# Optimization experiments

Measured on AMD Instinct MI355X. Metric: run time of the kernel, lower is better.

The kernel has to match this reference:

```python
import jax, jax.numpy as jnp
import numpy as np

B, T, D, U, C = 128, 256, 512, 1024, 10

def setup_inputs() -> dict:
    key = jax.random.key(0)
    ks = jax.random.split(key, 5)
    scale_in = 1.0 / np.sqrt(D)
    scale_rec = 1.0 / np.sqrt(U)
    return {
        "x": jax.random.normal(ks[0], (B, T, D), dtype=jnp.float32),
        "kernel": jax.random.normal(ks[1], (D, 4 * U), dtype=jnp.float32) * scale_in,
        "recurrent_kernel": jax.random.normal(ks[2], (U, 4 * U), dtype=jnp.float32) * scale_rec,
        "bias": jnp.zeros((4 * U,), dtype=jnp.float32),
        "w_cls": jax.random.normal(ks[3], (U, C), dtype=jnp.float32) * scale_rec,
        "b_cls": jnp.zeros((C,), dtype=jnp.float32),
    }

def _lstm_forward(x, kernel, recurrent_kernel, bias, w_cls, b_cls):
    # x: [B, T, D]. Keras LSTMCell gate order: i, f, g (candidate), o.
    # Precompute input projections for all timesteps in one big GEMM: [B,T,4U]
    xz = jnp.einsum('btd,dg->btg', x, kernel) + bias
    u = recurrent_kernel.shape[0]
    h0 = jnp.zeros((x.shape[0], u), dtype=x.dtype)
    c0 = jnp.zeros((x.shape[0], u), dtype=x.dtype)

    def step(carry, zt):
        h, c = carry
        z = zt + h @ recurrent_kernel          # [B, 4U]
        i, f, g, o = jnp.split(z, 4, axis=-1)
        i = jax.nn.sigmoid(i)
        f = jax.nn.sigmoid(f)
        o = jax.nn.sigmoid(o)
        c_new = f * c + i * jnp.tanh(g)
        h_new = o * jnp.tanh(c_new)
        return (h_new, c_new), None

    (h_last, _), _ = jax.lax.scan(step, (h0, c0), jnp.swapaxes(xz, 0, 1))
    logits = h_last @ w_cls + b_cls
    return jax.nn.softmax(logits, axis=-1)

def reference(x, kernel, recurrent_kernel, bias, w_cls, b_cls):
    return _lstm_forward(x, kernel, recurrent_kernel, bias, w_cls, b_cls)
```

## Files before the change

### kernel.cpp

```cpp
#include <hip/hip_runtime.h>

typedef unsigned short u16;
typedef unsigned int u32;
typedef unsigned long long u64;
typedef __attribute__((ext_vector_type(8))) short bf16x8;
typedef __attribute__((ext_vector_type(8))) unsigned short u16x8;
typedef __attribute__((ext_vector_type(4))) float f32x4;

#define TC 32
#define NCHUNK 8

static __device__ __forceinline__ u16 f2bf(float x) {
  union { float f; u32 u; } v; v.f = x;
  u32 r = v.u + 0x7fffu + ((v.u >> 16) & 1u);
  return (u16)(r >> 16);
}
static __device__ __forceinline__ float bf2f(u16 h) {
  union { u32 u; float f; } v; v.u = ((u32)h) << 16;
  return v.f;
}
static __device__ __forceinline__ float sigm(float x) {
  return 1.0f / (1.0f + __expf(-x));
}
static __device__ __forceinline__ void gload_lds16(const u16* g, u16* l) {
  __builtin_amdgcn_global_load_lds(
      (const __attribute__((address_space(1))) void*)g,
      (__attribute__((address_space(3))) void*)l, 16, 0, 0);
}

__global__ __launch_bounds__(256) void conv_x_kernel(const float* __restrict__ x,
                                                     u16* __restrict__ xh,
                                                     u16* __restrict__ xl) {
  int idx = blockIdx.x * 256 + threadIdx.x;
  size_t i8 = (size_t)idx * 8;
  int b = (int)(i8 >> 17);
  int r = (int)(i8 & 131071);
  int t = r >> 9;
  int d = r & 511;
  const f32x4* s = (const f32x4*)(x + i8);
  f32x4 v0 = s[0], v1 = s[1];
  u16x8 vh, vl;
#pragma unroll
  for (int j = 0; j < 8; ++j) {
    float v = (j < 4) ? v0[j] : v1[j - 4];
    u16 h = f2bf(v);
    vh[j] = h;
    vl[j] = f2bf(v - bf2f(h));
  }
  size_t o = ((size_t)(t * 128 + b)) * 512 + d;
  *(u16x8*)(xh + o) = vh;
  *(u16x8*)(xl + o) = vl;
}

__global__ __launch_bounds__(256) void tsplit_kernel(const float* __restrict__ w,
                                                     u16* __restrict__ oh,
                                                     u16* __restrict__ ol, int K) {
  int idx = blockIdx.x * 256 + threadIdx.x;
  int d = idx >> 10;
  int g4 = (idx & 1023) * 4;
  f32x4 v = *(const f32x4*)(w + (size_t)d * 4096 + g4);
#pragma unroll
  for (int j = 0; j < 4; ++j) {
    int g = g4 + j;
    u16 h = f2bf(v[j]);
    oh[(size_t)g * K + d] = h;
    ol[(size_t)g * K + d] = f2bf(v[j] - bf2f(h));
  }
}

__global__ __launch_bounds__(256) void gemm1_kernel(const u16* __restrict__ xh,
                                                    const u16* __restrict__ xl,
                                                    const u16* __restrict__ kh,
                                                    const u16* __restrict__ kl,
                                                    const float* __restrict__ bias,
                                                    float* __restrict__ xz, int c) {
  __shared__ u16 Ah[4096], Al[4096], Bh[4096], Bl[4096];
  const int tid = threadIdx.x;
  const int w = tid >> 6, l = tid & 63;
  const int m0w = blockIdx.y * 128;
  const int m0g = c * 4096 + m0w;
  const int n0 = blockIdx.x * 128;
  const int wr = w >> 1, wc = w & 1;
  const int srow = l >> 2, schunk = l & 3;
  const int fr = l & 15, fc = l >> 4;

  f32x4 acc[4][4];
#pragma unroll
  for (int a = 0; a < 4; ++a)
#pragma unroll
    for (int b = 0; b < 4; ++b) acc[a][b] = (f32x4){0.f, 0.f, 0.f, 0.f};

  for (int kt = 0; kt < 16; ++kt) {
    const int koff = kt * 32 + schunk * 8;
#pragma unroll
    for (int i = 0; i < 8; ++i) {
      const int q = w + i * 4;
      const int buf = q >> 3, ch = q & 7;
      const size_t ro = (size_t)(ch * 16 + srow);
      if (buf == 0)      gload_lds16(xh + (m0g + ro) * 512 + koff, Ah + ch * 512);
      else if (buf == 1) gload_lds16(xl + (m0g + ro) * 512 + koff, Al + ch * 512);
      else if (buf == 2) gload_lds16(kh + (n0 + ro) * 512 + koff, Bh + ch * 512);
      else               gload_lds16(kl + (n0 + ro) * 512 + koff, Bl + ch * 512);
    }
    __syncthreads();

    bf16x8 a_h[4], a_l[4], b_h[4], b_l[4];
#pragma unroll
    for (int mf = 0; mf < 4; ++mf) {
      int row = wr * 64 + mf * 16 + fr;
      a_h[mf] = *(const bf16x8*)(Ah + row * 32 + fc * 8);
      a_l[mf] = *(const bf16x8*)(Al + row * 32 + fc * 8);
    }
#pragma unroll
    for (int nf = 0; nf < 4; ++nf) {
      int col = wc * 64 + nf * 16 + fr;
      b_h[nf] = *(const bf16x8*)(Bh + col * 32 + fc * 8);
      b_l[nf] = *(const bf16x8*)(Bl + col * 32 + fc * 8);
    }
#pragma unroll
    for (int mf = 0; mf < 4; ++mf)
#pragma unroll
      for (int nf = 0; nf < 4; ++nf) {
        acc[mf][nf] = __builtin_amdgcn_mfma_f32_16x16x32_bf16(a_h[mf], b_h[nf], acc[mf][nf], 0, 0, 0);
        acc[mf][nf] = __builtin_amdgcn_mfma_f32_16x16x32_bf16(a_h[mf], b_l[nf], acc[mf][nf], 0, 0, 0);
        acc[mf][nf] = __builtin_amdgcn_mfma_f32_16x16x32_bf16(a_l[mf], b_h[nf], acc[mf][nf], 0, 0, 0);
      }
    __syncthreads();
  }

#pragma unroll
  for (int nf = 0; nf < 4; ++nf) {
    const int col = n0 + wc * 64 + nf * 16 + fr;
    const float bv = bias[col];
#pragma unroll
    for (int mf = 0; mf < 4; ++mf) {
      const int rw = m0w + wr * 64 + mf * 16 + fc * 4;
#pragma unroll
      for (int rg = 0; rg < 4; ++rg)
        xz[(size_t)(rw + rg) * 4096 + col] = acc[mf][nf][rg] + bv;
    }
  }
}

__global__ __launch_bounds__(256) void init_kernel(u32* flags) {
  for (int i = threadIdx.x; i < 4352; i += 256) flags[i] = 0u;
}

__global__ __launch_bounds__(256, 1) void lstm_scan_kernel(
    const float* __restrict__ xz,
    const u16* __restrict__ rwh, const u16* __restrict__ rwl,
    u32* __restrict__ h32, float* __restrict__ cf,
    u32* __restrict__ flags, int c) {
  __shared__ u16 Rh[32768];
  __shared__ u16 Rl[32768];
  const int tid = threadIdx.x;
  const int w = tid >> 6, l = tid & 63;
  const int blk = blockIdx.x;
  const int mi = blk >> 7, ui = blk & 127;

  for (int gidx = tid; gidx < 4096; gidx += 256) {
    const int lr = gidx & 63;
    const int ks = (gidx >> 6) & 31;
    const int nf = gidx >> 11;
    const int cc = lr & 15;
    const int kb = ks * 32 + ((lr >> 4) << 3);
    const int gate = nf * 2 + (cc >> 3);
    const size_t gcol = (size_t)(gate * 1024 + ui * 8 + (cc & 7));
    *(u16x8*)(Rh + gidx * 8) = *(const u16x8*)(rwh + gcol * 1024 + kb);
    *(u16x8*)(Rl + gidx * 8) = *(const u16x8*)(rwl + gcol * 1024 + kb);
  }

  const int fr = l & 15, fc = l >> 4;
  const int crow = mi * 64 + w * 16 + fc * 4;
  const int uu = ui * 8 + (fr & 7);
  const int gcol0 = ((fr >> 3) ? 1024 : 0) + uu;
  const int gcol1 = ((fr >> 3) ? 3072 : 2048) + uu;

  const u32 rbase = mi * 65536 + w * 16384 + l * 8;
  const u32 wbase = mi * 65536 + w * 16384 + (u32)(ui >> 2) * 512 +
                    ((u32)(ui & 3) * 16 + (u32)(fc * 4)) * 8 + (u32)(fr & 7);

  float cs[4] = {0.f, 0.f, 0.f, 0.f};
  if (c && fr < 8) {
#pragma unroll
    for (int rg = 0; rg < 4; ++rg) cs[rg] = cf[(size_t)(crow + rg) * 1024 + uu];
  }
  __syncthreads();

  for (int tc = 0; tc < TC; ++tc) {
    const int t = c * TC + tc;
    f32x4 a0 = (f32x4){0.f, 0.f, 0.f, 0.f};
    f32x4 a1 = (f32x4){0.f, 0.f, 0.f, 0.f};
    if (t) {
      const u32* hp = h32 + ((u32)(t & 1)) * 131072u + rbase;
#pragma unroll 4
      for (int ks = 0; ks < 32; ++ks) {
        const u64* hq = (const u64*)(hp + ks * 512);
        u64 q0 = __hip_atomic_load(hq + 0, __ATOMIC_RELAXED, __HIP_MEMORY_SCOPE_AGENT);
        u64 q1 = __hip_atomic_load(hq + 1, __ATOMIC_RELAXED, __HIP_MEMORY_SCOPE_AGENT);
        u64 q2 = __hip_atomic_load(hq + 2, __ATOMIC_RELAXED, __HIP_MEMORY_SCOPE_AGENT);
        u64 q3 = __hip_atomic_load(hq + 3, __ATOMIC_RELAXED, __HIP_MEMORY_SCOPE_AGENT);
        u32 P0 = (u32)q0, P1 = (u32)(q0 >> 32);
        u32 P2 = (u32)q1, P3 = (u32)(q1 >> 32);
        u32 P4 = (u32)q2, P5 = (u32)(q2 >> 32);
        u32 P6 = (u32)q3, P7 = (u32)(q3 >> 32);
        union { u32 wv[4]; bf16x8 v; } uh, ul;
        uh.wv[0] = __builtin_amdgcn_perm(P1, P0, 0x07060302u);
        ul.wv[0] = __builtin_amdgcn_perm(P1, P0, 0x05040100u);
        uh.wv[1] = __builtin_amdgcn_perm(P3, P2, 0x07060302u);
        ul.wv[1] = __builtin_amdgcn_perm(P3, P2, 0x05040100u);
        uh.wv[2] = __builtin_amdgcn_perm(P5, P4, 0x07060302u);
        ul.wv[2] = __builtin_amdgcn_perm(P5, P4, 0x05040100u);
        uh.wv[3] = __builtin_amdgcn_perm(P7, P6, 0x07060302u);
        ul.wv[3] = __builtin_amdgcn_perm(P7, P6, 0x05040100u);
        bf16x8 b0h = *(const bf16x8*)(Rh + (ks * 64 + l) * 8);
        bf16x8 b0l = *(const bf16x8*)(Rl + (ks * 64 + l) * 8);
        bf16x8 b1h = *(const bf16x8*)(Rh + ((32 + ks) * 64 + l) * 8);
        bf16x8 b1l = *(const bf16x8*)(Rl + ((32 + ks) * 64 + l) * 8);
        a0 = __builtin_amdgcn_mfma_f32_16x16x32_bf16(uh.v, b0h, a0, 0, 0, 0);
        a0 = __builtin_amdgcn_mfma_f32_16x16x32_bf16(uh.v, b0l, a0, 0, 0, 0);
        a0 = __builtin_amdgcn_mfma_f32_16x16x32_bf16(ul.v, b0h, a0, 0, 0, 0);
        a1 = __builtin_amdgcn_mfma_f32_16x16x32_bf16(uh.v, b1h, a1, 0, 0, 0);
        a1 = __builtin_amdgcn_mfma_f32_16x16x32_bf16(uh.v, b1l, a1, 0, 0, 0);
        a1 = __builtin_amdgcn_mfma_f32_16x16x32_bf16(ul.v, b1h, a1, 0, 0, 0);
      }
    }
    const float* xzt = xz + ((size_t)tc << 19);
    float z0[4], z1[4];
#pragma unroll
    for (int rg = 0; rg < 4; ++rg) {
      z0[rg] = a0[rg] + xzt[(size_t)(crow + rg) * 4096 + gcol0];
      z1[rg] = a1[rg] + xzt[(size_t)(crow + rg) * 4096 + gcol1];
    }
    u32* wp = h32 + ((u32)((t + 1) & 1)) * 131072u + wbase;
#pragma unroll
    for (int rg = 0; rg < 4; ++rg) {
      float p0 = __shfl_xor(z0[rg], 8, 64);
      float p1 = __shfl_xor(z1[rg], 8, 64);
      if (fr < 8) {
        float ig = sigm(z0[rg]);
        float fg = sigm(p0);
        float gg = tanhf(z1[rg]);
        float og = sigm(p1);
        float cn = fg * cs[rg] + ig * gg;
        cs[rg] = cn;
        float hv = og * tanhf(cn);
        u16 hi = f2bf(hv);
        u16 lo = f2bf(hv - bf2f(hi));
        u32 P = ((u32)hi << 16) | (u32)lo;
        __hip_atomic_store(wp + rg * 8, P,
                           __ATOMIC_RELAXED, __HIP_MEMORY_SCOPE_AGENT);
      }
    }
    const u32 tgt = (u32)(t + 1);
    asm volatile("s_waitcnt vmcnt(0)" ::: "memory");
    __syncthreads();
    u32* release = flags + 4096 + mi * 16;
    if (ui == 0) {
      if (tid == 0)
        __hip_atomic_store(flags + blk * 16, tgt, __ATOMIC_RELAXED, __HIP_MEMORY_SCOPE_AGENT);
      if (tid < 128) {
        const u32* f = flags + (mi * 128 + tid) * 16;
        for (int g = 0; g < (1 << 18); ++g) {
          if (__hip_atomic_load(f, __ATOMIC_RELAXED, __HIP_MEMORY_SCOPE_AGENT) >= tgt) break;
        }
      }
      __syncthreads();
      if (tid == 0)
        __hip_atomic_store(release, tgt, __ATOMIC_RELAXED, __HIP_MEMORY_SCOPE_AGENT);
    } else {
      if (tid == 0) {
        __hip_atomic_store(flags + blk * 16, tgt, __ATOMIC_RELAXED, __HIP_MEMORY_SCOPE_AGENT);
        for (int g = 0; g < (1 << 18); ++g) {
          if (__hip_atomic_load(release, __ATOMIC_RELAXED, __HIP_MEMORY_SCOPE_AGENT) >= tgt) break;
          __builtin_amdgcn_s_sleep(1);
        }
      }
      __syncthreads();
    }
  }

  if (fr < 8) {
#pragma unroll
    for (int rg = 0; rg < 4; ++rg) cf[(size_t)(crow + rg) * 1024 + uu] = cs[rg];
  }
}

__global__ __launch_bounds__(256) void cls_kernel(const u32* __restrict__ h32,
                                                  const float* __restrict__ wcls,
                                                  const float* __restrict__ bcls,
                                                  float* __restrict__ out) {
  __shared__ float red[2560];
  const int tid = threadIdx.x;
  const int row = blockIdx.x;
  const int rmi = row >> 6, rw = (row >> 4) & 3, lr = row & 15;
  const u32 rb = (u32)rmi * 65536u + (u32)rw * 16384u;
  float acc[10];
#pragma unroll
  for (int cc = 0; cc < 10; ++cc) acc[cc] = 0.f;
  const int k0 = tid * 4;
  for (int k = k0; k < k0 + 4; ++k) {
    const int ks = k >> 5, hi2 = (k >> 3) & 3, j = k & 7;
    u32 P = h32[rb + (u32)ks * 512u + ((u32)hi2 * 16u + (u32)lr) * 8u + (u32)j];
    float hv = bf2f((u16)(P >> 16)) + bf2f((u16)(P & 0xffffu));
#pragma unroll
    for (int cc = 0; cc < 10; ++cc) acc[cc] += hv * wcls[(size_t)k * 10 + cc];
  }
#pragma unroll
  for (int cc = 0; cc < 10; ++cc) red[tid * 10 + cc] = acc[cc];
  __syncthreads();
  for (int s = 128; s >= 1; s >>= 1) {
    if (tid < s) {
#pragma unroll
      for (int cc = 0; cc < 10; ++cc) red[tid * 10 + cc] += red[(tid + s) * 10 + cc];
    }
    __syncthreads();
  }
  if (tid == 0) {
    float lg[10];
    float m = -1e30f;
#pragma unroll
    for (int cc = 0; cc < 10; ++cc) { lg[cc] = red[cc] + bcls[cc]; m = fmaxf(m, lg[cc]); }
    float ssum = 0.f;
#pragma unroll
    for (int cc = 0; cc < 10; ++cc) { lg[cc] = __expf(lg[cc] - m); ssum += lg[cc]; }
    float inv = 1.f / ssum;
#pragma unroll
    for (int cc = 0; cc < 10; ++cc) out[row * 10 + cc] = lg[cc] * inv;
  }
}

extern "C" void kernel_launch(void* const* d_in, const int* in_sizes, int n_in,
                              void* d_out, int out_size, void* d_ws, size_t ws_size,
                              hipStream_t stream) {
  const float* x    = (const float*)d_in[0];
  const float* kern = (const float*)d_in[1];
  const float* rker = (const float*)d_in[2];
  const float* bias = (const float*)d_in[3];
  const float* wcls = (const float*)d_in[4];
  const float* bcls = (const float*)d_in[5];
  float* out = (float*)d_out;
  char* ws = (char*)d_ws;

  float* xz = (float*)(ws + 0UL);
  u16* xh   = (u16*)(ws + 67108864UL);
  u16* xl   = (u16*)(ws + 100663296UL);
  u16* kh   = (u16*)(ws + 134217728UL);
  u16* kl   = (u16*)(ws + 138412032UL);
  u16* rh   = (u16*)(ws + 142606336UL);
  u16* rl   = (u16*)(ws + 150994944UL);
  u32* h32  = (u32*)(ws + 159383552UL);
  float* cf = (float*)(ws + 160432128UL);
  u32* flg  = (u32*)(ws + 160956416UL);

  conv_x_kernel<<<8192, 256, 0, stream>>>(x, xh, xl);
  tsplit_kernel<<<2048, 256, 0, stream>>>(kern, kh, kl, 512);
  tsplit_kernel<<<4096, 256, 0, stream>>>(rker, rh, rl, 1024);
  init_kernel<<<1, 256, 0, stream>>>(flg);

  for (int c = 0; c < NCHUNK; ++c) {
    gemm1_kernel<<<dim3(32, 32), 256, 0, stream>>>(xh, xl, kh, kl, bias, xz, c);
    void* sargs[7];
    int cv = c;
    sargs[0] = (void*)&xz;
    sargs[1] = (void*)&rh;
    sargs[2] = (void*)&rl;
    sargs[3] = (void*)&h32;
    sargs[4] = (void*)&cf;
    sargs[5] = (void*)&flg;
    sargs[6] = (void*)&cv;
    hipLaunchCooperativeKernel((const void*)lstm_scan_kernel, dim3(256), dim3(256),
                               sargs, 0u, stream);
  }
  cls_kernel<<<128, 256, 0, stream>>>(h32, wcls, bcls, out);
}
```

Measured before the change: 4.270 ms.

## Store hidden state as single bf16 and drop low-part recurrent MFMA

```diff
diff --git a/kernel.cpp b/kernel.cpp
--- a/kernel.cpp
+++ b/kernel.cpp
@@ -149,7 +149,7 @@
 __global__ __launch_bounds__(256, 1) void lstm_scan_kernel(
     const float* __restrict__ xz,
     const u16* __restrict__ rwh, const u16* __restrict__ rwl,
-    u32* __restrict__ h32, float* __restrict__ cf,
+    u16* __restrict__ h16, float* __restrict__ cf,
     u32* __restrict__ flags, int c) {
   __shared__ u16 Rh[32768];
   __shared__ u16 Rl[32768];
@@ -189,50 +189,40 @@
 
   for (int tc = 0; tc < TC; ++tc) {
     const int t = c * TC + tc;
+    const float* xzt = xz + ((size_t)tc << 19);
+    float xv0[4], xv1[4];
+#pragma unroll
+    for (int rg = 0; rg < 4; ++rg) {
+      xv0[rg] = xzt[(size_t)(crow + rg) * 4096 + gcol0];
+      xv1[rg] = xzt[(size_t)(crow + rg) * 4096 + gcol1];
+    }
     f32x4 a0 = (f32x4){0.f, 0.f, 0.f, 0.f};
     f32x4 a1 = (f32x4){0.f, 0.f, 0.f, 0.f};
     if (t) {
-      const u32* hp = h32 + ((u32)(t & 1)) * 131072u + rbase;
+      const u16* hp = h16 + ((u32)(t & 1)) * 131072u + rbase;
 #pragma unroll 4
       for (int ks = 0; ks < 32; ++ks) {
         const u64* hq = (const u64*)(hp + ks * 512);
-        u64 q0 = __hip_atomic_load(hq + 0, __ATOMIC_RELAXED, __HIP_MEMORY_SCOPE_AGENT);
-        u64 q1 = __hip_atomic_load(hq + 1, __ATOMIC_RELAXED, __HIP_MEMORY_SCOPE_AGENT);
-        u64 q2 = __hip_atomic_load(hq + 2, __ATOMIC_RELAXED, __HIP_MEMORY_SCOPE_AGENT);
-        u64 q3 = __hip_atomic_load(hq + 3, __ATOMIC_RELAXED, __HIP_MEMORY_SCOPE_AGENT);
-        u32 P0 = (u32)q0, P1 = (u32)(q0 >> 32);
-        u32 P2 = (u32)q1, P3 = (u32)(q1 >> 32);
-        u32 P4 = (u32)q2, P5 = (u32)(q2 >> 32);
-        u32 P6 = (u32)q3, P7 = (u32)(q3 >> 32);
-        union { u32 wv[4]; bf16x8 v; } uh, ul;
-        uh.wv[0] = __builtin_amdgcn_perm(P1, P0, 0x07060302u);
-        ul.wv[0] = __builtin_amdgcn_perm(P1, P0, 0x05040100u);
-        uh.wv[1] = __builtin_amdgcn_perm(P3, P2, 0x07060302u);
-        ul.wv[1] = __builtin_amdgcn_perm(P3, P2, 0x05040100u);
-        uh.wv[2] = __builtin_amdgcn_perm(P5, P4, 0x07060302u);
-        ul.wv[2] = __builtin_amdgcn_perm(P5, P4, 0x05040100u);
-        uh.wv[3] = __builtin_amdgcn_perm(P7, P6, 0x07060302u);
-        ul.wv[3] = __builtin_amdgcn_perm(P7, P6, 0x05040100u);
+        union { u64 q[2]; bf16x8 v; } ah;
+        ah.q[0] = __hip_atomic_load(hq + 0, __ATOMIC_RELAXED, __HIP_MEMORY_SCOPE_AGENT);
+        ah.q[1] = __hip_atomic_load(hq + 1, __ATOMIC_RELAXED, __HIP_MEMORY_SCOPE_AGENT);
         bf16x8 b0h = *(const bf16x8*)(Rh + (ks * 64 + l) * 8);
         bf16x8 b0l = *(const bf16x8*)(Rl + (ks * 64 + l) * 8);
         bf16x8 b1h = *(const bf16x8*)(Rh + ((32 + ks) * 64 + l) * 8);
         bf16x8 b1l = *(const bf16x8*)(Rl + ((32 + ks) * 64 + l) * 8);
-        a0 = __builtin_amdgcn_mfma_f32_16x16x32_bf16(uh.v, b0h, a0, 0, 0, 0);
-        a0 = __builtin_amdgcn_mfma_f32_16x16x32_bf16(uh.v, b0l, a0, 0, 0, 0);
-        a0 = __builtin_amdgcn_mfma_f32_16x16x32_bf16(ul.v, b0h, a0, 0, 0, 0);
-        a1 = __builtin_amdgcn_mfma_f32_16x16x32_bf16(uh.v, b1h, a1, 0, 0, 0);
-        a1 = __builtin_amdgcn_mfma_f32_16x16x32_bf16(uh.v, b1l, a1, 0, 0, 0);
-        a1 = __builtin_amdgcn_mfma_f32_16x16x32_bf16(ul.v, b1h, a1, 0, 0, 0);
-      }
-    }
-    const float* xzt = xz + ((size_t)tc << 19);
+        a0 = __builtin_amdgcn_mfma_f32_16x16x32_bf16(ah.v, b0h, a0, 0, 0, 0);
+        a0 = __builtin_amdgcn_mfma_f32_16x16x32_bf16(ah.v, b0l, a0, 0, 0, 0);
+        a1 = __builtin_amdgcn_mfma_f32_16x16x32_bf16(ah.v, b1h, a1, 0, 0, 0);
+        a1 = __builtin_amdgcn_mfma_f32_16x16x32_bf16(ah.v, b1l, a1, 0, 0, 0);
+      }
+    }
     float z0[4], z1[4];
 #pragma unroll
     for (int rg = 0; rg < 4; ++rg) {
-      z0[rg] = a0[rg] + xzt[(size_t)(crow + rg) * 4096 + gcol0];
-      z1[rg] = a1[rg] + xzt[(size_t)(crow + rg) * 4096 + gcol1];
-    }
-    u32* wp = h32 + ((u32)((t + 1) & 1)) * 131072u + wbase;
+      z0[rg] = a0[rg] + xv0[rg];
+      z1[rg] = a1[rg] + xv1[rg];
+    }
+    u16* wp = h16 + ((u32)((t + 1) & 1)) * 131072u + wbase;
 #pragma unroll
     for (int rg = 0; rg < 4; ++rg) {
       float p0 = __shfl_xor(z0[rg], 8, 64);
@@ -245,10 +235,7 @@
         float cn = fg * cs[rg] + ig * gg;
         cs[rg] = cn;
         float hv = og * tanhf(cn);
-        u16 hi = f2bf(hv);
-        u16 lo = f2bf(hv - bf2f(hi));
-        u32 P = ((u32)hi << 16) | (u32)lo;
-        __hip_atomic_store(wp + rg * 8, P,
+        __hip_atomic_store(wp + rg * 8, f2bf(hv),
                            __ATOMIC_RELAXED, __HIP_MEMORY_SCOPE_AGENT);
       }
     }
@@ -286,7 +273,7 @@
   }
 }
 
-__global__ __launch_bounds__(256) void cls_kernel(const u32* __restrict__ h32,
+__global__ __launch_bounds__(256) void cls_kernel(const u16* __restrict__ h16,
                                                   const float* __restrict__ wcls,
                                                   const float* __restrict__ bcls,
                                                   float* __restrict__ out) {
@@ -301,8 +288,8 @@
   const int k0 = tid * 4;
   for (int k = k0; k < k0 + 4; ++k) {
     const int ks = k >> 5, hi2 = (k >> 3) & 3, j = k & 7;
-    u32 P = h32[rb + (u32)ks * 512u + ((u32)hi2 * 16u + (u32)lr) * 8u + (u32)j];
-    float hv = bf2f((u16)(P >> 16)) + bf2f((u16)(P & 0xffffu));
+    u16 P = h16[rb + (u32)ks * 512u + ((u32)hi2 * 16u + (u32)lr) * 8u + (u32)j];
+    float hv = bf2f(P);
 #pragma unroll
     for (int cc = 0; cc < 10; ++cc) acc[cc] += hv * wcls[(size_t)k * 10 + cc];
   }
@@ -349,9 +336,9 @@
   u16* kl   = (u16*)(ws + 138412032UL);
   u16* rh   = (u16*)(ws + 142606336UL);
   u16* rl   = (u16*)(ws + 150994944UL);
-  u32* h32  = (u32*)(ws + 159383552UL);
-  float* cf = (float*)(ws + 160432128UL);
-  u32* flg  = (u32*)(ws + 160956416UL);
+  u16* h16  = (u16*)(ws + 159383552UL);
+  float* cf = (float*)(ws + 159907840UL);
+  u32* flg  = (u32*)(ws + 160432128UL);
 
   conv_x_kernel<<<8192, 256, 0, stream>>>(x, xh, xl);
   tsplit_kernel<<<2048, 256, 0, stream>>>(kern, kh, kl, 512);
@@ -365,12 +352,12 @@
     sargs[0] = (void*)&xz;
     sargs[1] = (void*)&rh;
     sargs[2] = (void*)&rl;
-    sargs[3] = (void*)&h32;
+    sargs[3] = (void*)&h16;
     sargs[4] = (void*)&cf;
     sargs[5] = (void*)&flg;
     sargs[6] = (void*)&cv;
     hipLaunchCooperativeKernel((const void*)lstm_scan_kernel, dim3(256), dim3(256),
                                sargs, 0u, stream);
   }
-  cls_kernel<<<128, 256, 0, stream>>>(h32, wcls, bcls, out);
-}
+  cls_kernel<<<128, 256, 0, stream>>>(h16, wcls, bcls, out);
+}
```

Measured after the change: 4.049 ms. -5.2%, faster.
